# Kernel tuning notes

Measured on AMD Instinct MI355X. Metric: run time of the kernel, lower is better.

The kernel has to match this reference:

```python
import jax, jax.numpy as jnp
import numpy as np

EPS = 1e-8

def _cos_loss(a, b):
    # faithful to torch cos_loss: norm = sqrt(sum(x*x)), x / (norm + 1e-8)
    a_norm = jnp.sqrt(jnp.sum(a * a, axis=1, keepdims=True))
    b_norm = jnp.sqrt(jnp.sum(b * b, axis=1, keepdims=True))
    a_n = a / (a_norm + EPS)
    b_n = b / (b_norm + EPS)
    cossim = jnp.sum(a_n * b_n, axis=1)
    return jnp.mean(1.0 - cossim)

def setup_inputs() -> dict:
    key = jax.random.key(0)
    k1, k2, k3 = jax.random.split(key, 3)
    shape = (1, 768, 64, 64)  # [n, c_cat(block2 VGG16 feats), h, w]
    a = jax.random.normal(k1, shape, dtype=jnp.float32)
    b = jax.random.normal(k2, shape, dtype=jnp.float32)
    d = jax.random.normal(k3, shape, dtype=jnp.float32)
    return {"a": a, "b": b, "d": d}

def reference(a, b, d):
    n, c, h, w = a.shape
    hw = h * w
    a_flat = a.reshape(n, c, hw)   # [n, c, hw]
    b_flat = b.reshape(n, c, hw)   # [n, c, h2w2]
    d_flat = d.reshape(n, c, hw)
    # normalize exactly as argmin_cos_distance: sqrt(sum + 1e-8) then /(norm + 1e-8)
    b_norm = jnp.sqrt(jnp.sum(b_flat * b_flat, axis=1, keepdims=True) + EPS)
    b_n = b_flat / (b_norm + EPS)
    a_norm = jnp.sqrt(jnp.sum(a_flat * a_flat, axis=1, keepdims=True) + EPS)
    a_n = a_flat / (a_norm + EPS)
    # cosine distance matrix [n, hw, h2w2]
    d_mat = 1.0 - jnp.einsum('ncp,ncq->npq', a_n, b_n)
    z_best = jnp.argmin(d_mat, axis=2)  # [n, hw]
    # gather matched style features from d
    idx = jnp.broadcast_to(z_best[:, None, :], (n, c, hw))
    target_feats = jnp.take_along_axis(d_flat, idx, axis=2)  # [n, c, hw]
    # NNFM loss between rendered feats and matched style feats (score is detached)
    loss = _cos_loss(a_flat, target_feats)
    z_new = target_feats.reshape(n, c, h, w)
    return (loss, z_new, z_best)
```

## Files before the change

### kernel.cpp

```cpp
#include <hip/hip_runtime.h>
#include <math.h>

#define EPS  1e-8f
#define C    768
#define HW   4096
#define NKB  24
#define NNB  12
#define NBN  32
#define TAU  0.016f
#define NCH_NEW 12
#define NCH_OLD 48

typedef float  floatx4 __attribute__((ext_vector_type(4)));
typedef short  shortx8 __attribute__((ext_vector_type(8)));
typedef unsigned short ushort_t;
typedef unsigned int   uint_t;
typedef __attribute__((address_space(1))) uint_t as1_uint;
typedef __attribute__((address_space(3))) uint_t as3_uint;

__device__ __forceinline__ ushort_t f2bf(float v) {
    uint_t u = __float_as_uint(v);
    uint_t r = (u + 0x7FFFu + ((u >> 16) & 1u)) >> 16;
    return (ushort_t)r;
}
__device__ __forceinline__ void async_cp16(const ushort_t* g, ushort_t* l) {
    __builtin_amdgcn_global_load_lds((const as1_uint*)g, (as3_uint*)l, 16, 0, 0);
}

__global__ __launch_bounds__(256) void prep_kernel(
    const float* __restrict__ a, const float* __restrict__ b,
    const float* __restrict__ d,
    ushort_t* __restrict__ Ah, ushort_t* __restrict__ Bh,
    float* __restrict__ dT, float* __restrict__ bT,
    float* __restrict__ nbp2, float* __restrict__ out)
{
    __shared__ float tile[64][65];
    const int t = threadIdx.x;
    const int p0 = blockIdx.x * 64;
    const int c0 = blockIdx.y * 64;
    const int x = t & 63, y4 = t >> 6;
    const int pl = t >> 2, g = t & 3;
    const int pg = p0 + pl;
    const int sw = (pg >> 1) & 3;

    if (blockIdx.x == 0 && blockIdx.y == 0 && t == 0) out[0] = 0.f;

#pragma unroll
    for (int i = 0; i < 16; ++i) {
        int c = y4 * 16 + i;
        tile[c][x] = d[(size_t)(c0 + c) * HW + p0 + x];
    }
    __syncthreads();
#pragma unroll
    for (int i = 0; i < 16; ++i) {
        int p = y4 * 16 + i;
        dT[(size_t)(p0 + p) * C + c0 + x] = tile[x][p];
    }
    __syncthreads();

#pragma unroll
    for (int i = 0; i < 16; ++i) {
        int c = y4 * 16 + i;
        tile[c][x] = b[(size_t)(c0 + c) * HW + p0 + x];
    }
    __syncthreads();
#pragma unroll
    for (int i = 0; i < 16; ++i) {
        int p = y4 * 16 + i;
        bT[(size_t)(p0 + p) * C + c0 + x] = tile[x][p];
    }
#pragma unroll
    for (int h = 0; h < 2; ++h) {
        const int kb = (c0 >> 5) + h;
        uint_t w[4];
#pragma unroll
        for (int u = 0; u < 4; ++u) {
            ushort_t lo = f2bf(tile[h * 32 + g * 8 + 2 * u][pl]);
            ushort_t hi = f2bf(tile[h * 32 + g * 8 + 2 * u + 1][pl]);
            w[u] = (uint_t)lo | ((uint_t)hi << 16);
        }
        uint4* oh = (uint4*)(Bh + ((size_t)kb * HW + pg) * 32);
        oh[g ^ sw] = make_uint4(w[0], w[1], w[2], w[3]);
    }
    if (t < 64) {
        float s = 0.f;
#pragma unroll
        for (int c = 0; c < 64; ++c) { float v = tile[c][t]; s += v * v; }
        nbp2[blockIdx.y * HW + p0 + t] = s;
    }
    __syncthreads();

#pragma unroll
    for (int i = 0; i < 16; ++i) {
        int c = y4 * 16 + i;
        tile[c][x] = a[(size_t)(c0 + c) * HW + p0 + x];
    }
    __syncthreads();
#pragma unroll
    for (int h = 0; h < 2; ++h) {
        const int kb = (c0 >> 5) + h;
        uint_t w[4];
#pragma unroll
        for (int u = 0; u < 4; ++u) {
            ushort_t lo = f2bf(tile[h * 32 + g * 8 + 2 * u][pl]);
            ushort_t hi = f2bf(tile[h * 32 + g * 8 + 2 * u + 1][pl]);
            w[u] = (uint_t)lo | ((uint_t)hi << 16);
        }
        uint4* oh = (uint4*)(Ah + ((size_t)kb * HW + pg) * 32);
        oh[g ^ sw] = make_uint4(w[0], w[1], w[2], w[3]);
    }
}

__global__ __launch_bounds__(256, 4) void gemm_mfma_kernel(
    const ushort_t* __restrict__ Ah, const ushort_t* __restrict__ Bh,
    const float* __restrict__ nbp2,
    float* __restrict__ pv1, int* __restrict__ pi1,
    float* __restrict__ pv2, int* __restrict__ pi2)
{
    __shared__ __align__(16) char smem[16896];
    ushort_t* sA  = (ushort_t*)smem;
    ushort_t* sB  = (ushort_t*)(smem + 8192);
    float*    nb_s = (float*)(smem + 16384);

    const int tid  = threadIdx.x;
    const int lane = tid & 63;
    const int wave = tid >> 6;
    const int wm = wave >> 1, wn = wave & 1;
    const int bm = blockIdx.x, bn = blockIdx.y;
    const int l15 = lane & 15, l4 = lane >> 4;
    const int swz = (l15 >> 1) & 3;

    if (tid < 128) {
        float s = 0.f;
        int q = bn * 128 + tid;
#pragma unroll
        for (int ch = 0; ch < NNB; ++ch) s += nbp2[ch * HW + q];
        nb_s[tid] = 1.0f / (sqrtf(s + EPS) + EPS);
    }

    floatx4 acc[4][4];
#pragma unroll
    for (int i = 0; i < 4; ++i)
#pragma unroll
        for (int j = 0; j < 4; ++j) acc[i][j] = (floatx4){0.f, 0.f, 0.f, 0.f};

    for (int kb = 0; kb < NKB; ++kb) {
        const size_t aoff = (size_t)(kb * HW + bm * 128) * 32 + tid * 8;
        const size_t boff = (size_t)(kb * HW + bn * 128) * 32 + tid * 8;
        async_cp16(Ah + aoff,        sA + tid * 8);
        async_cp16(Ah + aoff + 2048, sA + tid * 8 + 2048);
        async_cp16(Bh + boff,        sB + tid * 8);
        async_cp16(Bh + boff + 2048, sB + tid * 8 + 2048);
        __syncthreads();

        shortx8 af[4], bf_[4];
#pragma unroll
        for (int i = 0; i < 4; ++i)
            af[i] = *(const shortx8*)&sA[((wm * 4 + i) * 16 + l15) * 32 + ((l4 ^ swz) * 8)];
#pragma unroll
        for (int j = 0; j < 4; ++j)
            bf_[j] = *(const shortx8*)&sB[((wn * 4 + j) * 16 + l15) * 32 + ((l4 ^ swz) * 8)];
#pragma unroll
        for (int i = 0; i < 4; ++i)
#pragma unroll
            for (int j = 0; j < 4; ++j)
                acc[i][j] = __builtin_amdgcn_mfma_f32_16x16x32_bf16(af[i], bf_[j], acc[i][j], 0, 0, 0);
        __syncthreads();
    }

    float rnb[4];
#pragma unroll
    for (int j = 0; j < 4; ++j)
        rnb[j] = nb_s[wn * 64 + j * 16 + l15];

    float* lv1 = (float*)smem;
    int*   li1 = (int*)(smem + 1024);
    float* lv2 = (float*)(smem + 2048);
    int*   li2 = (int*)(smem + 3072);

#pragma unroll
    for (int i = 0; i < 4; ++i) {
#pragma unroll
        for (int r = 0; r < 4; ++r) {
            float v1 = -INFINITY, v2 = -INFINITY; int i1 = 0, i2 = 0;
#pragma unroll
            for (int j = 0; j < 4; ++j) {
                float sv = acc[i][j][r] * rnb[j];
                int q = bn * 128 + wn * 64 + j * 16 + l15;
                if (sv > v1) { v2 = v1; i2 = i1; v1 = sv; i1 = q; }
                else if (sv > v2) { v2 = sv; i2 = q; }
            }
#pragma unroll
            for (int m = 1; m < 16; m <<= 1) {
                float ov1 = __shfl_xor(v1, m, 64);
                int   oi1 = __shfl_xor(i1, m, 64);
                float ov2 = __shfl_xor(v2, m, 64);
                int   oi2 = __shfl_xor(i2, m, 64);
                if (ov1 > v1 || (ov1 == v1 && oi1 < i1)) {
                    if (v1 > ov2 || (v1 == ov2 && i1 < oi2)) { v2 = v1; i2 = i1; }
                    else { v2 = ov2; i2 = oi2; }
                    v1 = ov1; i1 = oi1;
                } else if (ov1 > v2 || (ov1 == v2 && oi1 < i2)) {
                    v2 = ov1; i2 = oi1;
                }
            }
            if (l15 == 0) {
                int pl = wm * 64 + i * 16 + l4 * 4 + r;
                lv1[pl * 2 + wn] = v1; li1[pl * 2 + wn] = i1;
                lv2[pl * 2 + wn] = v2; li2[pl * 2 + wn] = i2;
            }
        }
    }
    __syncthreads();
    if (tid < 128) {
        float v1 = lv1[tid * 2],     v2 = lv2[tid * 2];
        int   i1 = li1[tid * 2],     i2 = li2[tid * 2];
        float w1 = lv1[tid * 2 + 1], w2 = lv2[tid * 2 + 1];
        int   j1 = li1[tid * 2 + 1], j2 = li2[tid * 2 + 1];
        if (w1 > v1 || (w1 == v1 && j1 < i1)) {
            if (v1 > w2 || (v1 == w2 && i1 < j2)) { v2 = v1; i2 = i1; }
            else { v2 = w2; i2 = j2; }
            v1 = w1; i1 = j1;
        } else if (w1 > v2 || (w1 == v2 && j1 < i2)) {
            v2 = w1; i2 = j1;
        }
        int p = bm * 128 + tid;
        pv1[p * NBN + bn] = v1; pi1[p * NBN + bn] = i1;
        pv2[p * NBN + bn] = v2; pi2[p * NBN + bn] = i2;
    }
}

__global__ __launch_bounds__(256) void reduce_recheck_kernel(
    const float* __restrict__ a, const float* __restrict__ b,
    const float* __restrict__ bT, int bt_ok,
    const float* __restrict__ pv1, const int* __restrict__ pi1,
    const float* __restrict__ pv2, const int* __restrict__ pi2,
    int* __restrict__ zb, float* __restrict__ out_zbest)
{
    const int wave = threadIdx.x >> 6, lane = threadIdx.x & 63;
    const int p = blockIdx.x * 4 + wave;
    const int tq = lane & 31;

    float v1, v2; int i1, cand;
    if (lane < 32) {
        v1 = pv1[p * NBN + tq]; i1 = pi1[p * NBN + tq]; v2 = pv2[p * NBN + tq];
        cand = i1;
    } else {
        v1 = -INFINITY; v2 = -INFINITY; i1 = 0x7fffffff;
        cand = pi2[p * NBN + tq];
    }
#pragma unroll
    for (int m = 1; m < 32; m <<= 1) {
        float ov1 = __shfl_xor(v1, m, 64);
        int   oi1 = __shfl_xor(i1, m, 64);
        float ov2 = __shfl_xor(v2, m, 64);
        if (ov1 > v1 || (ov1 == v1 && oi1 < i1)) {
            v2 = fmaxf(v1, ov2); v1 = ov1; i1 = oi1;
        } else {
            v2 = fmaxf(v2, ov1);
        }
    }
    v1 = __shfl(v1, 0, 64); v2 = __shfl(v2, 0, 64); i1 = __shfl(i1, 0, 64);

    if (v1 - v2 >= TAU) {
        if (lane == 0) { zb[p] = i1; out_zbest[p] = (float)i1; }
        return;
    }

    int q = cand;
    float dot = 0.f, b2 = 0.f;
    if (bt_ok) {
        const float* br = bT + (size_t)q * C;
        const float* ap = a + p;
#pragma unroll 4
        for (int c = 0; c < C; c += 4) {
            float4 bv = *(const float4*)(br + c);
            dot += ap[(size_t)c * HW] * bv.x + ap[(size_t)(c + 1) * HW] * bv.y
                 + ap[(size_t)(c + 2) * HW] * bv.z + ap[(size_t)(c + 3) * HW] * bv.w;
            b2  += bv.x * bv.x + bv.y * bv.y + bv.z * bv.z + bv.w * bv.w;
        }
    } else {
#pragma unroll 8
        for (int c = 0; c < C; ++c) {
            float av = a[c * HW + p];
            float bv = b[c * HW + q];
            dot += av * bv; b2 += bv * bv;
        }
    }
    float s = dot / (sqrtf(b2 + EPS) + EPS);
#pragma unroll
    for (int m = 1; m < 64; m <<= 1) {
        float os = __shfl_xor(s, m, 64);
        int   oq = __shfl_xor(q, m, 64);
        if (os > s || (os == s && oq < q)) { s = os; q = oq; }
    }
    if (lane == 0) { zb[p] = q; out_zbest[p] = (float)q; }
}

__global__ __launch_bounds__(256) void gather_loss_kernel(
    const float* __restrict__ a, const float* __restrict__ dT,
    const int* __restrict__ zb, float* __restrict__ out,
    float* __restrict__ pdot, float* __restrict__ pa2, float* __restrict__ pt2)
{
    __shared__ float tile[64][65];
    __shared__ int qs[64];
    const int t = threadIdx.x;
    const int p0 = blockIdx.x * 64;
    const int c0 = blockIdx.y * 64;
    if (t < 64) qs[t] = zb[p0 + t];
    __syncthreads();

    {
        const int pl = t >> 2, sub = t & 3;
        const float* src = dT + (size_t)qs[pl] * C + c0 + sub * 16;
        float4 v0 = *(const float4*)(src);
        float4 v1 = *(const float4*)(src + 4);
        float4 v2 = *(const float4*)(src + 8);
        float4 v3 = *(const float4*)(src + 12);
        float* dst = &tile[pl][sub * 16];
        dst[0] = v0.x; dst[1] = v0.y; dst[2]  = v0.z; dst[3]  = v0.w;
        dst[4] = v1.x; dst[5] = v1.y; dst[6]  = v1.z; dst[7]  = v1.w;
        dst[8] = v2.x; dst[9] = v2.y; dst[10] = v2.z; dst[11] = v2.w;
        dst[12] = v3.x; dst[13] = v3.y; dst[14] = v3.z; dst[15] = v3.w;
    }
    __syncthreads();

    const int p = t & 63, cg = t >> 6;
    float dot = 0.f, a2 = 0.f, t2 = 0.f;
#pragma unroll
    for (int i = 0; i < 16; ++i) {
        int cc = cg * 16 + i;
        float tv = tile[p][cc];
        float av = a[(size_t)(c0 + cc) * HW + p0 + p];
        out[1 + (size_t)(c0 + cc) * HW + p0 + p] = tv;
        dot += av * tv; a2 += av * av; t2 += tv * tv;
    }
    __shared__ float r1[256], r2[256], r3[256];
    r1[t] = dot; r2[t] = a2; r3[t] = t2;
    __syncthreads();
    if (t < 64) {
        dot = r1[t] + r1[t + 64] + r1[t + 128] + r1[t + 192];
        a2  = r2[t] + r2[t + 64] + r2[t + 128] + r2[t + 192];
        t2  = r3[t] + r3[t + 64] + r3[t + 128] + r3[t + 192];
        pdot[blockIdx.y * HW + p0 + t] = dot;
        pa2[blockIdx.y * HW + p0 + t]  = a2;
        pt2[blockIdx.y * HW + p0 + t]  = t2;
    }
}

__global__ __launch_bounds__(256) void loss_finalize_kernel(
    const float* __restrict__ pdot, const float* __restrict__ pa2,
    const float* __restrict__ pt2, float* __restrict__ out, int nch)
{
    int p = blockIdx.x * 256 + threadIdx.x;
    float dot = 0.f, a2 = 0.f, t2 = 0.f;
#pragma unroll 12
    for (int ch = 0; ch < nch; ++ch) {
        dot += pdot[ch * HW + p];
        a2  += pa2[ch * HW + p];
        t2  += pt2[ch * HW + p];
    }
    float cs = dot / ((sqrtf(a2) + EPS) * (sqrtf(t2) + EPS));
    float contrib = 1.f - cs;
    __shared__ float red[256];
    red[threadIdx.x] = contrib;
    __syncthreads();
    for (int s = 128; s > 0; s >>= 1) {
        if (threadIdx.x < s) red[threadIdx.x] += red[threadIdx.x + s];
        __syncthreads();
    }
    if (threadIdx.x == 0) atomicAdd(out, red[0] * (1.0f / HW));
}

__global__ __launch_bounds__(256) void bnorm_partial_fb_kernel(
    const float* __restrict__ b, float* __restrict__ nbp)
{
    int q = blockIdx.x * 256 + threadIdx.x;
    int c0 = blockIdx.y * 32;
    float s = 0.f;
#pragma unroll 8
    for (int c = c0; c < c0 + 32; ++c) { float v = b[c * HW + q]; s += v * v; }
    nbp[blockIdx.y * HW + q] = s;
}

__global__ __launch_bounds__(256) void bnorm_finalize_fb_kernel(
    const float* __restrict__ nbp, float* __restrict__ nb)
{
    int q = blockIdx.x * 256 + threadIdx.x;
    float s = 0.f;
#pragma unroll
    for (int ch = 0; ch < NKB; ++ch) s += nbp[ch * HW + q];
    nb[q] = sqrtf(s + EPS) + EPS;
}

__global__ __launch_bounds__(256) void gemm_argmax_fb_kernel(
    const float* __restrict__ A, const float* __restrict__ B,
    const float* __restrict__ nb,
    float* __restrict__ pval, int* __restrict__ pidx)
{
    __shared__ __align__(16) char smem[16384];
    float (*As)[128] = (float (*)[128])smem;
    float (*Bs)[128] = (float (*)[128])(smem + 4096);
    const int m0 = blockIdx.x * 128, q0 = blockIdx.y * 128;
    const int tid = threadIdx.x;
    const int tx = tid & 15, ty = tid >> 4;
    const int lr = tid >> 5, lc = (tid & 31) * 4;
    float acc[8][8] = {};
    for (int k0 = 0; k0 < C; k0 += 8) {
        *(float4*)&As[lr][lc] = *(const float4*)&A[(k0 + lr) * HW + m0 + lc];
        *(float4*)&Bs[lr][lc] = *(const float4*)&B[(k0 + lr) * HW + q0 + lc];
        __syncthreads();
#pragma unroll
        for (int kk = 0; kk < 8; ++kk) {
            float a8[8], b8[8];
            *(float4*)&a8[0] = *(float4*)&As[kk][ty * 8];
            *(float4*)&a8[4] = *(float4*)&As[kk][ty * 8 + 4];
            *(float4*)&b8[0] = *(float4*)&Bs[kk][tx * 8];
            *(float4*)&b8[4] = *(float4*)&Bs[kk][tx * 8 + 4];
#pragma unroll
            for (int i = 0; i < 8; ++i)
#pragma unroll
                for (int j = 0; j < 8; ++j) acc[i][j] += a8[i] * b8[j];
        }
        __syncthreads();
    }
    float nbv[8];
#pragma unroll
    for (int j = 0; j < 8; ++j) nbv[j] = nb[q0 + tx * 8 + j];
    float (*rv)[16] = (float (*)[16])smem;
    int   (*ri)[16] = (int   (*)[16])(smem + 8192);
#pragma unroll
    for (int i = 0; i < 8; ++i) {
        float bv = -INFINITY; int bi = 0;
#pragma unroll
        for (int j = 0; j < 8; ++j) {
            float s = acc[i][j] / nbv[j];
            int q = q0 + tx * 8 + j;
            if (s > bv) { bv = s; bi = q; }
        }
        rv[ty * 8 + i][tx] = bv;
        ri[ty * 8 + i][tx] = bi;
    }
    __syncthreads();
    if (tid < 128) {
        float bv = rv[tid][0]; int bi = ri[tid][0];
#pragma unroll
        for (int t = 1; t < 16; ++t) {
            float v = rv[tid][t]; int ii = ri[tid][t];
            if (v > bv || (v == bv && ii < bi)) { bv = v; bi = ii; }
        }
        pval[(m0 + tid) * NBN + blockIdx.y] = bv;
        pidx[(m0 + tid) * NBN + blockIdx.y] = bi;
    }
}

__global__ __launch_bounds__(256) void reduce_fb_kernel(
    const float* __restrict__ pval, const int* __restrict__ pidx,
    int* __restrict__ zb, float* __restrict__ out_zbest)
{
    int p = blockIdx.x * 256 + threadIdx.x;
    float bv = pval[p * NBN]; int bi = pidx[p * NBN];
#pragma unroll 8
    for (int t = 1; t < NBN; ++t) {
        float v = pval[p * NBN + t]; int ii = pidx[p * NBN + t];
        if (v > bv || (v == bv && ii < bi)) { bv = v; bi = ii; }
    }
    zb[p] = bi;
    out_zbest[p] = (float)bi;
}

__global__ __launch_bounds__(256) void gather_partial_kernel(
    const float* __restrict__ a, const float* __restrict__ d,
    const int* __restrict__ zb, float* __restrict__ out,
    float* __restrict__ pdot, float* __restrict__ pa2, float* __restrict__ pt2)
{
    int p = blockIdx.x * 256 + threadIdx.x;
    int ch = blockIdx.y;
    int c0 = ch * (C / NCH_OLD);
    int q = zb[p];
    float dot = 0.f, a2 = 0.f, t2 = 0.f;
#pragma unroll
    for (int c = c0; c < c0 + C / NCH_OLD; ++c) {
        float av = a[c * HW + p];
        float tv = d[c * HW + q];
        dot += av * tv; a2 += av * av; t2 += tv * tv;
        out[1 + c * HW + p] = tv;
    }
    pdot[ch * HW + p] = dot;
    pa2[ch * HW + p] = a2;
    pt2[ch * HW + p] = t2;
}

extern "C" void kernel_launch(void* const* d_in, const int* in_sizes, int n_in,
                              void* d_out, int out_size, void* d_ws, size_t ws_size,
                              hipStream_t stream) {
    const float* a = (const float*)d_in[0];
    const float* b = (const float*)d_in[1];
    const float* d = (const float*)d_in[2];
    float* out = (float*)d_out;
    float* out_zbest = out + 1 + (size_t)C * HW;

    char* ws = (char*)d_ws;
    size_t off = 0;
    auto alloc = [&](size_t bytes) { void* p = ws + off; off = (off + bytes + 255) & ~(size_t)255; return p; };

    const size_t PACK = (size_t)C * HW * 2;
    ushort_t* Ah = (ushort_t*)alloc(PACK);
    ushort_t* Bh = (ushort_t*)alloc(PACK);
    float* nbp = (float*)alloc((size_t)NKB * HW * 4);
    float* pv1 = (float*)alloc((size_t)HW * NBN * 4);
    int*   pi1 = (int*)alloc((size_t)HW * NBN * 4);
    float* pv2 = (float*)alloc((size_t)HW * NBN * 4);
    int*   pi2 = (int*)alloc((size_t)HW * NBN * 4);
    int*   zb  = (int*)alloc(HW * 4);
    float* pdot = (float*)alloc((size_t)NCH_NEW * HW * 4);
    float* pa2  = (float*)alloc((size_t)NCH_NEW * HW * 4);
    float* pt2  = (float*)alloc((size_t)NCH_NEW * HW * 4);
    float* dT  = (float*)alloc((size_t)C * HW * 4);
    float* bT  = (float*)alloc((size_t)C * HW * 4);
    bool fast = off <= ws_size;

    if (fast) {
        prep_kernel<<<dim3(HW / 64, C / 64), 256, 0, stream>>>(
            a, b, d, Ah, Bh, dT, bT, nbp, out);
        gemm_mfma_kernel<<<dim3(HW / 128, HW / 128), 256, 0, stream>>>(
            Ah, Bh, nbp, pv1, pi1, pv2, pi2);
        reduce_recheck_kernel<<<HW / 4, 256, 0, stream>>>(
            a, b, bT, 1, pv1, pi1, pv2, pi2, zb, out_zbest);
        gather_loss_kernel<<<dim3(HW / 64, NCH_NEW), 256, 0, stream>>>(
            a, dT, zb, out, pdot, pa2, pt2);
        loss_finalize_kernel<<<HW / 256, 256, 0, stream>>>(pdot, pa2, pt2, out, NCH_NEW);
    } else {
        off = 0;
        float* nb = (float*)alloc(HW * 4);
        nbp = (float*)alloc((size_t)NKB * HW * 4);
        pv1 = (float*)alloc((size_t)HW * NBN * 4);
        pi1 = (int*)alloc((size_t)HW * NBN * 4);
        zb  = (int*)alloc(HW * 4);
        float* pdot2 = (float*)alloc((size_t)NCH_OLD * HW * 4);
        float* pa22  = (float*)alloc((size_t)NCH_OLD * HW * 4);
        float* pt22  = (float*)alloc((size_t)NCH_OLD * HW * 4);
        hipMemsetAsync(d_out, 0, sizeof(float), stream);
        bnorm_partial_fb_kernel<<<dim3(HW / 256, NKB), 256, 0, stream>>>(b, nbp);
        bnorm_finalize_fb_kernel<<<HW / 256, 256, 0, stream>>>(nbp, nb);
        gemm_argmax_fb_kernel<<<dim3(HW / 128, HW / 128), 256, 0, stream>>>(a, b, nb, pv1, pi1);
        reduce_fb_kernel<<<HW / 256, 256, 0, stream>>>(pv1, pi1, zb, out_zbest);
        gather_partial_kernel<<<dim3(HW / 256, NCH_OLD), 256, 0, stream>>>(
            a, d, zb, out, pdot2, pa22, pt22);
        loss_finalize_kernel<<<HW / 256, 256, 0, stream>>>(pdot2, pa22, pt22, out, NCH_OLD);
    }
}
```

Baseline: 178.3 us.

## Split prep kernel across tensors and fuse argmax recheck into gather kernel

The prep kernel gains a z grid dimension so the d, b and a tensors are transposed and packed by separate blocks instead of serially within one block, giving more parallelism. The reduce/recheck kernel is removed and its per-pixel candidate reduction and fp32 recheck are folded into the gather kernel, which now resolves the best index for its 64 pixels before gathering. This removes one launch and the zb round trip. In exchange, the recheck is redundantly recomputed by each of the 12 channel-block slices of the gather grid, and pixels are handled serially per wave.

```diff
diff --git a/kernel.cpp b/kernel.cpp
--- a/kernel.cpp
+++ b/kernel.cpp
@@ -8,7 +8,6 @@
 #define NNB  12
 #define NBN  32
 #define TAU  0.016f
-#define NCH_NEW 12
 #define NCH_OLD 48
 
 typedef float  floatx4 __attribute__((ext_vector_type(4)));
@@ -38,76 +37,58 @@
     const int t = threadIdx.x;
     const int p0 = blockIdx.x * 64;
     const int c0 = blockIdx.y * 64;
+    const int z  = blockIdx.z;
     const int x = t & 63, y4 = t >> 6;
-    const int pl = t >> 2, g = t & 3;
-    const int pg = p0 + pl;
-    const int sw = (pg >> 1) & 3;
-
-    if (blockIdx.x == 0 && blockIdx.y == 0 && t == 0) out[0] = 0.f;
-
+
+    if (z == 0 && blockIdx.x == 0 && blockIdx.y == 0 && t == 0) out[0] = 0.f;
+
+    const float* src = (z == 0) ? d : (z == 1 ? b : a);
 #pragma unroll
     for (int i = 0; i < 16; ++i) {
         int c = y4 * 16 + i;
-        tile[c][x] = d[(size_t)(c0 + c) * HW + p0 + x];
-    }
-    __syncthreads();
-#pragma unroll
-    for (int i = 0; i < 16; ++i) {
-        int p = y4 * 16 + i;
-        dT[(size_t)(p0 + p) * C + c0 + x] = tile[x][p];
-    }
-    __syncthreads();
-
-#pragma unroll
-    for (int i = 0; i < 16; ++i) {
-        int c = y4 * 16 + i;
-        tile[c][x] = b[(size_t)(c0 + c) * HW + p0 + x];
-    }
-    __syncthreads();
-#pragma unroll
-    for (int i = 0; i < 16; ++i) {
-        int p = y4 * 16 + i;
-        bT[(size_t)(p0 + p) * C + c0 + x] = tile[x][p];
-    }
-#pragma unroll
-    for (int h = 0; h < 2; ++h) {
-        const int kb = (c0 >> 5) + h;
-        uint_t w[4];
-#pragma unroll
-        for (int u = 0; u < 4; ++u) {
-            ushort_t lo = f2bf(tile[h * 32 + g * 8 + 2 * u][pl]);
-            ushort_t hi = f2bf(tile[h * 32 + g * 8 + 2 * u + 1][pl]);
-            w[u] = (uint_t)lo | ((uint_t)hi << 16);
-        }
-        uint4* oh = (uint4*)(Bh + ((size_t)kb * HW + pg) * 32);
-        oh[g ^ sw] = make_uint4(w[0], w[1], w[2], w[3]);
-    }
-    if (t < 64) {
-        float s = 0.f;
-#pragma unroll
-        for (int c = 0; c < 64; ++c) { float v = tile[c][t]; s += v * v; }
-        nbp2[blockIdx.y * HW + p0 + t] = s;
-    }
-    __syncthreads();
-
-#pragma unroll
-    for (int i = 0; i < 16; ++i) {
-        int c = y4 * 16 + i;
-        tile[c][x] = a[(size_t)(c0 + c) * HW + p0 + x];
-    }
-    __syncthreads();
-#pragma unroll
-    for (int h = 0; h < 2; ++h) {
-        const int kb = (c0 >> 5) + h;
-        uint_t w[4];
-#pragma unroll
-        for (int u = 0; u < 4; ++u) {
-            ushort_t lo = f2bf(tile[h * 32 + g * 8 + 2 * u][pl]);
-            ushort_t hi = f2bf(tile[h * 32 + g * 8 + 2 * u + 1][pl]);
-            w[u] = (uint_t)lo | ((uint_t)hi << 16);
-        }
-        uint4* oh = (uint4*)(Ah + ((size_t)kb * HW + pg) * 32);
-        oh[g ^ sw] = make_uint4(w[0], w[1], w[2], w[3]);
+        tile[c][x] = src[(size_t)(c0 + c) * HW + p0 + x];
+    }
+    __syncthreads();
+
+    if (z == 0) {
+#pragma unroll
+        for (int i = 0; i < 16; ++i) {
+            int p = y4 * 16 + i;
+            dT[(size_t)(p0 + p) * C + c0 + x] = tile[x][p];
+        }
+        return;
+    }
+    if (z == 1) {
+#pragma unroll
+        for (int i = 0; i < 16; ++i) {
+            int p = y4 * 16 + i;
+            bT[(size_t)(p0 + p) * C + c0 + x] = tile[x][p];
+        }
+        if (t < 64) {
+            float s = 0.f;
+#pragma unroll
+            for (int c = 0; c < 64; ++c) { float v = tile[c][t]; s += v * v; }
+            nbp2[blockIdx.y * HW + p0 + t] = s;
+        }
+    }
+    {
+        const int pl = t >> 2, g = t & 3;
+        const int pg = p0 + pl;
+        const int sw = (pg >> 1) & 3;
+        ushort_t* dst = (z == 1) ? Bh : Ah;
+#pragma unroll
+        for (int h = 0; h < 2; ++h) {
+            const int kb = (c0 >> 5) + h;
+            uint_t w[4];
+#pragma unroll
+            for (int u = 0; u < 4; ++u) {
+                ushort_t lo = f2bf(tile[h * 32 + g * 8 + 2 * u][pl]);
+                ushort_t hi = f2bf(tile[h * 32 + g * 8 + 2 * u + 1][pl]);
+                w[u] = (uint_t)lo | ((uint_t)hi << 16);
+            }
+            uint4* oh = (uint4*)(dst + ((size_t)kb * HW + pg) * 32);
+            oh[g ^ sw] = make_uint4(w[0], w[1], w[2], w[3]);
+        }
     }
 }
 
@@ -230,84 +211,74 @@
     }
 }
 
-__global__ __launch_bounds__(256) void reduce_recheck_kernel(
-    const float* __restrict__ a, const float* __restrict__ b,
-    const float* __restrict__ bT, int bt_ok,
+__global__ __launch_bounds__(256) void gather_finish_kernel(
+    const float* __restrict__ a, const float* __restrict__ bT,
+    const float* __restrict__ dT,
     const float* __restrict__ pv1, const int* __restrict__ pi1,
     const float* __restrict__ pv2, const int* __restrict__ pi2,
-    int* __restrict__ zb, float* __restrict__ out_zbest)
-{
-    const int wave = threadIdx.x >> 6, lane = threadIdx.x & 63;
-    const int p = blockIdx.x * 4 + wave;
-    const int tq = lane & 31;
-
-    float v1, v2; int i1, cand;
-    if (lane < 32) {
-        v1 = pv1[p * NBN + tq]; i1 = pi1[p * NBN + tq]; v2 = pv2[p * NBN + tq];
-        cand = i1;
-    } else {
-        v1 = -INFINITY; v2 = -INFINITY; i1 = 0x7fffffff;
-        cand = pi2[p * NBN + tq];
-    }
-#pragma unroll
-    for (int m = 1; m < 32; m <<= 1) {
-        float ov1 = __shfl_xor(v1, m, 64);
-        int   oi1 = __shfl_xor(i1, m, 64);
-        float ov2 = __shfl_xor(v2, m, 64);
-        if (ov1 > v1 || (ov1 == v1 && oi1 < i1)) {
-            v2 = fmaxf(v1, ov2); v1 = ov1; i1 = oi1;
-        } else {
-            v2 = fmaxf(v2, ov1);
-        }
-    }
-    v1 = __shfl(v1, 0, 64); v2 = __shfl(v2, 0, 64); i1 = __shfl(i1, 0, 64);
-
-    if (v1 - v2 >= TAU) {
-        if (lane == 0) { zb[p] = i1; out_zbest[p] = (float)i1; }
-        return;
-    }
-
-    int q = cand;
-    float dot = 0.f, b2 = 0.f;
-    if (bt_ok) {
-        const float* br = bT + (size_t)q * C;
-        const float* ap = a + p;
-#pragma unroll 4
-        for (int c = 0; c < C; c += 4) {
-            float4 bv = *(const float4*)(br + c);
-            dot += ap[(size_t)c * HW] * bv.x + ap[(size_t)(c + 1) * HW] * bv.y
-                 + ap[(size_t)(c + 2) * HW] * bv.z + ap[(size_t)(c + 3) * HW] * bv.w;
-            b2  += bv.x * bv.x + bv.y * bv.y + bv.z * bv.z + bv.w * bv.w;
-        }
-    } else {
-#pragma unroll 8
-        for (int c = 0; c < C; ++c) {
-            float av = a[c * HW + p];
-            float bv = b[c * HW + q];
-            dot += av * bv; b2 += bv * bv;
-        }
-    }
-    float s = dot / (sqrtf(b2 + EPS) + EPS);
-#pragma unroll
-    for (int m = 1; m < 64; m <<= 1) {
-        float os = __shfl_xor(s, m, 64);
-        int   oq = __shfl_xor(q, m, 64);
-        if (os > s || (os == s && oq < q)) { s = os; q = oq; }
-    }
-    if (lane == 0) { zb[p] = q; out_zbest[p] = (float)q; }
-}
-
-__global__ __launch_bounds__(256) void gather_loss_kernel(
-    const float* __restrict__ a, const float* __restrict__ dT,
-    const int* __restrict__ zb, float* __restrict__ out,
+    float* __restrict__ out,
     float* __restrict__ pdot, float* __restrict__ pa2, float* __restrict__ pt2)
 {
     __shared__ float tile[64][65];
     __shared__ int qs[64];
     const int t = threadIdx.x;
+    const int wv = t >> 6, lane = t & 63;
     const int p0 = blockIdx.x * 64;
     const int c0 = blockIdx.y * 64;
-    if (t < 64) qs[t] = zb[p0 + t];
+    float* out_zbest = out + 1 + (size_t)C * HW;
+
+    for (int r = 0; r < 16; ++r) {
+        const int pl = wv * 16 + r;
+        const int p = p0 + pl;
+        const int tq = lane & 31;
+        float v1, v2; int i1, cand;
+        if (lane < 32) {
+            v1 = pv1[p * NBN + tq]; i1 = pi1[p * NBN + tq]; v2 = pv2[p * NBN + tq];
+            cand = i1;
+        } else {
+            v1 = -INFINITY; v2 = -INFINITY; i1 = 0x7fffffff;
+            cand = pi2[p * NBN + tq];
+        }
+#pragma unroll
+        for (int m = 1; m < 32; m <<= 1) {
+            float ov1 = __shfl_xor(v1, m, 64);
+            int   oi1 = __shfl_xor(i1, m, 64);
+            float ov2 = __shfl_xor(v2, m, 64);
+            if (ov1 > v1 || (ov1 == v1 && oi1 < i1)) {
+                v2 = fmaxf(v1, ov2); v1 = ov1; i1 = oi1;
+            } else {
+                v2 = fmaxf(v2, ov1);
+            }
+        }
+        v1 = __shfl(v1, 0, 64); v2 = __shfl(v2, 0, 64); i1 = __shfl(i1, 0, 64);
+
+        int zq = i1;
+        if (v1 - v2 < TAU) {
+            int q = cand;
+            float dot = 0.f, b2 = 0.f;
+            const float* br = bT + (size_t)q * C;
+            const float* ap = a + p;
+#pragma unroll 4
+            for (int c = 0; c < C; c += 4) {
+                float4 bv = *(const float4*)(br + c);
+                dot += ap[(size_t)c * HW] * bv.x + ap[(size_t)(c + 1) * HW] * bv.y
+                     + ap[(size_t)(c + 2) * HW] * bv.z + ap[(size_t)(c + 3) * HW] * bv.w;
+                b2  += bv.x * bv.x + bv.y * bv.y + bv.z * bv.z + bv.w * bv.w;
+            }
+            float s = dot / (sqrtf(b2 + EPS) + EPS);
+#pragma unroll
+            for (int m = 1; m < 64; m <<= 1) {
+                float os = __shfl_xor(s, m, 64);
+                int   oq = __shfl_xor(q, m, 64);
+                if (os > s || (os == s && oq < q)) { s = os; q = oq; }
+            }
+            zq = q;
+        }
+        if (lane == 0) {
+            qs[pl] = zq;
+            if (blockIdx.y == 0) out_zbest[p] = (float)zq;
+        }
+    }
     __syncthreads();
 
     {
@@ -512,31 +483,28 @@
     int*   pi1 = (int*)alloc((size_t)HW * NBN * 4);
     float* pv2 = (float*)alloc((size_t)HW * NBN * 4);
     int*   pi2 = (int*)alloc((size_t)HW * NBN * 4);
-    int*   zb  = (int*)alloc(HW * 4);
-    float* pdot = (float*)alloc((size_t)NCH_NEW * HW * 4);
-    float* pa2  = (float*)alloc((size_t)NCH_NEW * HW * 4);
-    float* pt2  = (float*)alloc((size_t)NCH_NEW * HW * 4);
+    float* pdot = (float*)alloc((size_t)NNB * HW * 4);
+    float* pa2  = (float*)alloc((size_t)NNB * HW * 4);
+    float* pt2  = (float*)alloc((size_t)NNB * HW * 4);
     float* dT  = (float*)alloc((size_t)C * HW * 4);
     float* bT  = (float*)alloc((size_t)C * HW * 4);
     bool fast = off <= ws_size;
 
     if (fast) {
-        prep_kernel<<<dim3(HW / 64, C / 64), 256, 0, stream>>>(
+        prep_kernel<<<dim3(HW / 64, C / 64, 3), 256, 0, stream>>>(
             a, b, d, Ah, Bh, dT, bT, nbp, out);
         gemm_mfma_kernel<<<dim3(HW / 128, HW / 128), 256, 0, stream>>>(
             Ah, Bh, nbp, pv1, pi1, pv2, pi2);
-        reduce_recheck_kernel<<<HW / 4, 256, 0, stream>>>(
-            a, b, bT, 1, pv1, pi1, pv2, pi2, zb, out_zbest);
-        gather_loss_kernel<<<dim3(HW / 64, NCH_NEW), 256, 0, stream>>>(
-            a, dT, zb, out, pdot, pa2, pt2);
-        loss_finalize_kernel<<<HW / 256, 256, 0, stream>>>(pdot, pa2, pt2, out, NCH_NEW);
+        gather_finish_kernel<<<dim3(HW / 64, NNB), 256, 0, stream>>>(
+            a, bT, dT, pv1, pi1, pv2, pi2, out, pdot, pa2, pt2);
+        loss_finalize_kernel<<<HW / 256, 256, 0, stream>>>(pdot, pa2, pt2, out, NNB);
     } else {
         off = 0;
         float* nb = (float*)alloc(HW * 4);
         nbp = (float*)alloc((size_t)NKB * HW * 4);
         pv1 = (float*)alloc((size_t)HW * NBN * 4);
         pi1 = (int*)alloc((size_t)HW * NBN * 4);
-        zb  = (int*)alloc(HW * 4);
+        int* zb = (int*)alloc(HW * 4);
         float* pdot2 = (float*)alloc((size_t)NCH_OLD * HW * 4);
         float* pa22  = (float*)alloc((size_t)NCH_OLD * HW * 4);
         float* pt22  = (float*)alloc((size_t)NCH_OLD * HW * 4);
```

Measured after the change: 308.2 us. 1.73x slower.
